# Optimization experiments

Measured on AMD Instinct MI355X. Metric: run time of the kernel, lower is better.

The kernel has to match this reference:

```python
import jax, jax.numpy as jnp
import numpy as np
from jax import lax

DIM = 192
HEADS = 8


def conv3d(x, w, b, groups=1, pad=0):
    # x: [B,C,T,H,W], w: [O, C//groups, kt, kh, kw]
    out = lax.conv_general_dilated(
        x, w, window_strides=(1, 1, 1),
        padding=[(pad, pad)] * 3,
        dimension_numbers=('NCDHW', 'OIDHW', 'NCDHW'),
        feature_group_count=groups)
    return out + b[None, :, None, None, None]


def setup_inputs() -> dict:
    key = jax.random.key(0)
    ks = jax.random.split(key, 8)
    d = DIM
    x = jax.random.normal(ks[0], (2, d, 8, 64, 64), dtype=jnp.float32)
    qkv_w = jax.random.normal(ks[1], (3 * d, d, 1, 1, 1), dtype=jnp.float32) * 0.02
    qkv_b = jnp.zeros((3 * d,), dtype=jnp.float32)
    dw_w = jax.random.normal(ks[2], (3 * d, 1, 3, 3, 3), dtype=jnp.float32) * 0.02
    dw_b = jnp.zeros((3 * d,), dtype=jnp.float32)
    temperature = jnp.ones((HEADS, 1, 1), dtype=jnp.float32)
    proj_w = jax.random.normal(ks[3], (d, d, 1, 1, 1), dtype=jnp.float32) * 0.02
    proj_b = jnp.zeros((d,), dtype=jnp.float32)
    return {"x": x, "qkv_w": qkv_w, "qkv_b": qkv_b, "dw_w": dw_w,
            "dw_b": dw_b, "temperature": temperature,
            "proj_w": proj_w, "proj_b": proj_b}


def reference(x, qkv_w, qkv_b, dw_w, dw_b, temperature, proj_w, proj_b):
    b, c, t, h, w = x.shape
    head_dim = c // HEADS
    n = t * h * w
    qkv = conv3d(x, qkv_w, qkv_b)                      # [b, 3c, t, h, w]
    qkv = conv3d(qkv, dw_w, dw_b, groups=3 * c, pad=1)  # depthwise 3x3x3
    q, k, v = jnp.split(qkv, 3, axis=1)
    def to_heads(z):
        return z.reshape(b, HEADS, head_dim, n)         # b head c (thw)
    q, k, v = to_heads(q), to_heads(k), to_heads(v)
    # L2 normalize along token axis (F.normalize, eps=1e-12)
    q = q / jnp.maximum(jnp.linalg.norm(q, axis=-1, keepdims=True), 1e-12)
    k = k / jnp.maximum(jnp.linalg.norm(k, axis=-1, keepdims=True), 1e-12)
    attn = jnp.einsum('bhcn,bhdn->bhcd', q, k) * temperature  # [b,H,hd,hd]
    attn = jax.nn.softmax(attn, axis=-1)
    out = jnp.einsum('bhcd,bhdn->bhcn', attn, v)        # [b,H,hd,n]
    out = out.reshape(b, c, t, h, w)
    return conv3d(out, proj_w, proj_b)
```

## Files before the change

### kernel.cpp

```cpp
#include <hip/hip_runtime.h>

#define NTOK 32768
#define CIN 192
#define C3 576
#define HEADS 8
#define HD 24

typedef __attribute__((ext_vector_type(8))) short bf16x8;
typedef __attribute__((ext_vector_type(16))) float f32x16;
typedef __attribute__((ext_vector_type(4))) unsigned int u32x4;

__device__ __forceinline__ float bf2f(unsigned int u) {
  union { unsigned int i; float f; } x; x.i = u << 16; return x.f;
}
__device__ __forceinline__ unsigned short f2bf(float f) {
  union { float f; unsigned int i; } x; x.f = f;
  unsigned int r = x.i + 0x7fffu + ((x.i >> 16) & 1u);
  return (unsigned short)(r >> 16);
}

__global__ __launch_bounds__(256) void k_wfrag(const float* __restrict__ W,
                                               unsigned short* __restrict__ Wf,
                                               int nchunk) {
  const int g = blockIdx.x * 256 + threadIdx.x;
  if (g >= nchunk) return;
  const int ol = g & 63, hi = (g >> 6) & 1, kk = (g >> 7) % 12, ot = g / 1536;
  const float* src = W + (size_t)(ot * 64 + ol) * CIN + kk * 16 + hi * 8;
  bf16x8 p;
#pragma unroll
  for (int e = 0; e < 8; ++e) p[e] = (short)f2bf(src[e]);
  *(bf16x8*)&Wf[(size_t)g * 8] = p;
}

__device__ __forceinline__ void issue12(bf16x8 (&a)[12],
                                        const unsigned short* p) {
#pragma unroll
  for (int kk = 0; kk < 12; ++kk) {
    unsigned long long ad = (unsigned long long)(p + kk * 1024);
    asm volatile("global_load_dwordx4 %0, %1, off" : "=v"(a[kk]) : "v"(ad));
  }
}

template<int XBF, int OUTF32>
__global__ __launch_bounds__(256, 2) void k_gemm_rr(
    const void* __restrict__ Xv, const unsigned short* __restrict__ Wf0,
    const float* __restrict__ bias, void* __restrict__ Yv, int ot_per,
    long xbs, long ybs, long wbs)
{
  __shared__ __align__(16) unsigned short Xf[12 * 128 * 8];
  const int tid = threadIdx.x;
  const int b = blockIdx.z;
  const int n0 = blockIdx.x * 64;
  const unsigned short* Wf = Wf0 + (size_t)b * wbs;
  const int lsub = tid & 15;

  if (XBF) {
    const unsigned short* X = (const unsigned short*)Xv + (size_t)b * xbs;
#pragma unroll
    for (int i = 0; i < 12; ++i) {
      const int g = tid + i * 256;
      const int c = g >> 4, nq = (g & 15) * 4;
      unsigned short t4[4];
      *(unsigned long long*)t4 =
          *(const unsigned long long*)&X[(size_t)c * NTOK + n0 + nq];
      const int chunk = (c >> 4) * 128 + ((c >> 3) & 1) * 64 + nq;
      const int e = c & 7;
#pragma unroll
      for (int s = 0; s < 4; ++s) {
        const int le = (s + lsub) & 3;
        Xf[(chunk + le) * 8 + e] = t4[le];
      }
    }
  } else {
    const float* X = (const float*)Xv + (size_t)b * xbs;
#pragma unroll
    for (int i = 0; i < 12; ++i) {
      const int g = tid + i * 256;
      const int c = g >> 4, nq = (g & 15) * 4;
      float4 v = *(const float4*)&X[(size_t)c * NTOK + n0 + nq];
      float vv[4] = {v.x, v.y, v.z, v.w};
      const int chunk = (c >> 4) * 128 + ((c >> 3) & 1) * 64 + nq;
      const int e = c & 7;
#pragma unroll
      for (int s = 0; s < 4; ++s) {
        const int le = (s + lsub) & 3;
        Xf[(chunk + le) * 8 + e] = f2bf(vv[le]);
      }
    }
  }
  __syncthreads();

  const int lane = tid & 63;
  const int wv = tid >> 6;
  const int o_w = (wv >> 1) * 32;
  const int n_w = (wv & 1) * 32;
  const int j = lane & 31;
  const int hi = lane >> 5;

  bf16x8 bfr[12];
#pragma unroll
  for (int kk = 0; kk < 12; ++kk)
    bfr[kk] = *(const bf16x8*)&Xf[(kk * 128 + hi * 64 + n_w + j) * 8];

  const unsigned short* wbase = Wf + ((size_t)hi * 64 + o_w + j) * 8;

  auto tile = [&](bf16x8 (&a)[12], int o0) {
    f32x16 acc0, acc1;
#pragma unroll
    for (int i = 0; i < 16; ++i) { acc0[i] = 0.f; acc1[i] = 0.f; }
#pragma unroll
    for (int kp = 0; kp < 6; ++kp) {
      acc0 = __builtin_amdgcn_mfma_f32_32x32x16_bf16(a[2 * kp], bfr[2 * kp], acc0, 0, 0, 0);
      acc1 = __builtin_amdgcn_mfma_f32_32x32x16_bf16(a[2 * kp + 1], bfr[2 * kp + 1], acc1, 0, 0, 0);
    }
    if (OUTF32) {
      float* Y = (float*)Yv + (size_t)b * ybs;
#pragma unroll
      for (int r = 0; r < 16; ++r) {
        const int row = o_w + (r & 3) + 8 * (r >> 2) + 4 * hi;
        Y[(size_t)(o0 + row) * NTOK + n0 + n_w + j] =
            acc0[r] + acc1[r] + bias[o0 + row];
      }
    } else {
      unsigned short* Y = (unsigned short*)Yv + (size_t)b * ybs;
#pragma unroll
      for (int r = 0; r < 16; ++r) {
        const int row = o_w + (r & 3) + 8 * (r >> 2) + 4 * hi;
        Y[(size_t)(o0 + row) * NTOK + n0 + n_w + j] =
            f2bf(acc0[r] + acc1[r] + bias[o0 + row]);
      }
    }
  };

  bf16x8 aA[12], aB[12];
  issue12(aA, wbase);
  asm volatile("s_waitcnt vmcnt(0)" ::: "memory");
  __builtin_amdgcn_sched_barrier(0);

  int it = 0;
  while (true) {
    if (it + 1 < ot_per) issue12(aB, wbase + (size_t)(it + 1) * 12288);
    tile(aA, it * 64);
    if (it + 1 >= ot_per) break;
    asm volatile("s_waitcnt vmcnt(16)" ::: "memory");
    __builtin_amdgcn_sched_barrier(0);
    ++it;
    if (it + 1 < ot_per) issue12(aA, wbase + (size_t)(it + 1) * 12288);
    tile(aB, it * 64);
    if (it + 1 >= ot_per) break;
    asm volatile("s_waitcnt vmcnt(16)" ::: "memory");
    __builtin_amdgcn_sched_barrier(0);
    ++it;
  }
}

__global__ __launch_bounds__(256, 2) void k_dwconv(
    const unsigned short* __restrict__ in0,
    const float* __restrict__ wdw,
    const float* __restrict__ bdw,
    unsigned short* __restrict__ out0)
{
  __shared__ __align__(16) unsigned short s[8][18][76];
  const int tid = threadIdx.x;
  const int ch = blockIdx.y;
  const int h0 = blockIdx.x * 16;
  const size_t boff = (size_t)blockIdx.z * C3 * NTOK;
  const unsigned short* inch = in0 + boff + (size_t)ch * NTOK;

  for (int r = tid; r < 144; r += 256) {
    const int t = r / 18, rr = r % 18;
    s[t][rr][7] = 0;
    s[t][rr][72] = 0;
  }
  for (int idx = tid; idx < 144 * 8; idx += 256) {
    const int row = idx >> 3, seg = idx & 7;
    const int t = row / 18, rr = row % 18;
    const int h = h0 + rr - 1;
    u32x4 v = {0u, 0u, 0u, 0u};
    if (h >= 0 && h < 64)
      v = *(const u32x4*)&inch[t * 4096 + h * 64 + seg * 8];
    *(u32x4*)&s[t][rr][8 + seg * 8] = v;
  }
  float wr[27];
#pragma unroll
  for (int i = 0; i < 27; ++i) wr[i] = wdw[ch * 27 + i];
  const float bias = bdw[ch];
  __syncthreads();

  const int wloc = tid & 63;
  const int hl0 = (tid >> 6) * 4;
  float acc[8][4];
#pragma unroll
  for (int t = 0; t < 8; ++t)
#pragma unroll
    for (int i = 0; i < 4; ++i) acc[t][i] = 0.f;

#pragma unroll
  for (int tt = 0; tt < 8; ++tt) {
    float v[6][3];
#pragma unroll
    for (int r = 0; r < 6; ++r)
#pragma unroll
      for (int c = 0; c < 3; ++c)
        v[r][c] = bf2f(s[tt][hl0 + r][7 + wloc + c]);
#pragma unroll
    for (int p = 0; p < 3; ++p) {
      const int t = tt + 1 - p;
      if (t < 0 || t > 7) continue;
#pragma unroll
      for (int hi = 0; hi < 4; ++hi) {
        float a = 0.f;
#pragma unroll
        for (int dh = 0; dh < 3; ++dh)
#pragma unroll
          for (int dw = 0; dw < 3; ++dw)
            a += wr[p * 9 + dh * 3 + dw] * v[hi + dh][dw];
        acc[t][hi] += a;
      }
    }
  }

  unsigned short* outch = out0 + boff + (size_t)ch * NTOK;
#pragma unroll
  for (int t = 0; t < 8; ++t)
#pragma unroll
    for (int hi = 0; hi < 4; ++hi)
      outch[t * 4096 + (h0 + hl0 + hi) * 64 + wloc] = f2bf(acc[t][hi] + bias);
}

__global__ __launch_bounds__(256) void k_gram(
    const unsigned short* __restrict__ post0, float* __restrict__ Sp0)
{
  const int tid = threadIdx.x;
  const int h = blockIdx.y;
  const unsigned short* post = post0 + (size_t)blockIdx.z * C3 * NTOK;
  float* Sp = Sp0 + (size_t)blockIdx.z * HEADS * 32 * 640;
  const int lane = tid & 63;
  const int wv = tid >> 6;
  const int c = lane & 31;
  const int off = (lane >> 5) * 8;
  const unsigned short* q = post + (size_t)(h * HD + c) * NTOK;
  const unsigned short* k = post + (size_t)(192 + h * HD + c) * NTOK;

  __shared__ float Sl[24][25];
  __shared__ float nl[48];
  for (int i = tid; i < 600; i += 256) ((float*)Sl)[i] = 0.f;
  if (tid < 48) nl[tid] = 0.f;
  __syncthreads();

  f32x16 acc;
#pragma unroll
  for (int i = 0; i < 16; ++i) acc[i] = 0.f;
  float sqq = 0.f, sqk = 0.f;

  const int base = blockIdx.x * 1024 + wv * 256 + off;
#pragma unroll
  for (int i = 0; i < 16; ++i) {
    const int n = base + i * 16;
    bf16x8 a = *(const bf16x8*)&q[n];
    bf16x8 b = *(const bf16x8*)&k[n];
#pragma unroll
    for (int e = 0; e < 8; ++e) {
      float fa = bf2f((unsigned short)a[e]);
      float fb = bf2f((unsigned short)b[e]);
      sqq += fa * fa;
      sqk += fb * fb;
    }
    acc = __builtin_amdgcn_mfma_f32_32x32x16_bf16(a, b, acc, 0, 0, 0);
  }

  sqq += __shfl_down(sqq, 32, 64);
  sqk += __shfl_down(sqk, 32, 64);
  if (lane < 32 && c < 24) {
    atomicAdd(&nl[c], sqq);
    atomicAdd(&nl[24 + c], sqk);
  }
  if (c < 24) {
#pragma unroll
    for (int r = 0; r < 16; ++r) {
      const int row = (r & 3) + 8 * (r >> 2) + 4 * (lane >> 5);
      if (row < 24) atomicAdd(&Sl[row][c], acc[r]);
    }
  }
  __syncthreads();
  float* outp = Sp + ((size_t)h * 32 + blockIdx.x) * 640;
  for (int i = tid; i < 576; i += 256) outp[i] = Sl[i / 24][i % 24];
  if (tid < 48) outp[576 + tid] = nl[tid];
}

__global__ __launch_bounds__(256) void k_attn_wfrag(
    const float* __restrict__ Sp0, const float* __restrict__ temp,
    const float* __restrict__ projw, unsigned short* __restrict__ wfc0)
{
  const int h = blockIdx.x;
  const int tid = threadIdx.x;
  const float* base = Sp0 + (size_t)blockIdx.y * HEADS * 32 * 640 +
                      (size_t)h * 32 * 640;
  unsigned short* wfc = wfc0 + (size_t)blockIdx.y * 3 * 1536 * 8;

  __shared__ float Ssum[24][25];
  __shared__ float attn[24][25];
  __shared__ float nqs[24], nks[24];

  for (int i = tid; i < 576; i += 256) {
    float a = 0.f;
#pragma unroll 4
    for (int ch = 0; ch < 32; ++ch) a += base[(size_t)ch * 640 + i];
    Ssum[i / 24][i % 24] = a;
  }
  if (tid < 48) {
    float a = 0.f;
#pragma unroll 4
    for (int ch = 0; ch < 32; ++ch) a += base[(size_t)ch * 640 + 576 + tid];
    float nv = fmaxf(sqrtf(a), 1e-12f);
    if (tid < 24) nqs[tid] = nv; else nks[tid - 24] = nv;
  }
  __syncthreads();
  if (tid < 24) {
    const int c = tid;
    const float tmp = temp[h];
    float row[24];
    float m = -1e30f;
#pragma unroll
    for (int d = 0; d < 24; ++d) {
      float v = Ssum[c][d] / (nqs[c] * nks[d]) * tmp;
      row[d] = v;
      m = fmaxf(m, v);
    }
    float ssum = 0.f;
#pragma unroll
    for (int d = 0; d < 24; ++d) { float e = __expf(row[d] - m); row[d] = e; ssum += e; }
    const float inv = 1.f / ssum;
#pragma unroll
    for (int d = 0; d < 24; ++d) attn[c][d] = row[d] * inv;
  }
  __syncthreads();
  for (int e = tid; e < 192 * 24; e += 256) {
    const int o = e / 24, d = e % 24;
    float a = 0.f;
#pragma unroll
    for (int c = 0; c < 24; ++c) a += projw[o * 192 + h * 24 + c] * attn[c][d];
    const int c2 = h * 24 + d;
    const int ot = o >> 6, ol = o & 63;
    const int kk = c2 >> 4, hi = (c2 >> 3) & 1, e2 = c2 & 7;
    wfc[(size_t)((((ot * 12 + kk) * 2 + hi) * 64) + ol) * 8 + e2] = f2bf(a);
  }
}

extern "C" void kernel_launch(void* const* d_in, const int* in_sizes, int n_in,
                              void* d_out, int out_size, void* d_ws, size_t ws_size,
                              hipStream_t stream) {
  const float* x      = (const float*)d_in[0];
  const float* qkv_w  = (const float*)d_in[1];
  const float* qkv_b  = (const float*)d_in[2];
  const float* dw_w   = (const float*)d_in[3];
  const float* dw_b   = (const float*)d_in[4];
  const float* temp   = (const float*)d_in[5];
  const float* proj_w = (const float*)d_in[6];
  const float* proj_b = (const float*)d_in[7];
  float* out = (float*)d_out;

  char* ws = (char*)d_ws;
  size_t off = 0;
  unsigned short* post = (unsigned short*)(ws + off);
  off += (size_t)2 * C3 * NTOK * sizeof(unsigned short);
  unsigned short* pre = (unsigned short*)(ws + off);
  off += (size_t)2 * C3 * NTOK * sizeof(unsigned short);
  float* Sp = (float*)(ws + off);
  off += (size_t)2 * HEADS * 32 * 640 * sizeof(float);
  off = (off + 255) & ~(size_t)255;
  unsigned short* wfq = (unsigned short*)(ws + off);
  off += (size_t)9 * 1536 * 8 * sizeof(unsigned short);
  unsigned short* wfc = (unsigned short*)(ws + off);
  off += (size_t)2 * 3 * 1536 * 8 * sizeof(unsigned short);

  k_wfrag<<<54, 256, 0, stream>>>(qkv_w, wfq, 9 * 1536);

  k_gemm_rr<0, 0><<<dim3(512, 1, 2), 256, 0, stream>>>(
      x, wfq, qkv_b, pre, 9, (long)CIN * NTOK, (long)C3 * NTOK, 0);

  k_dwconv<<<dim3(4, C3, 2), 256, 0, stream>>>(pre, dw_w, dw_b, post);

  k_gram<<<dim3(32, HEADS, 2), 256, 0, stream>>>(post, Sp);

  k_attn_wfrag<<<dim3(HEADS, 2), 256, 0, stream>>>(Sp, temp, proj_w, wfc);

  k_gemm_rr<1, 1><<<dim3(512, 1, 2), 256, 0, stream>>>(
      post + (size_t)384 * NTOK, wfc, proj_b, out, 3,
      (long)C3 * NTOK, (long)CIN * NTOK, (long)3 * 1536 * 8);
}
```

Baseline: 153.6 us.

## Split GEMM output channels across blocks with XCD-aware block remapping

Both pointwise GEMMs are relaunched with three times as many blocks. Each block now covers one third of the output-channel tiles (three tiles for the QKV GEMM, one for the projection) instead of all of them. Block IDs are remapped so the three blocks sharing a token tile land on the same XCD and can reuse the X tile in that XCD's L2. This raises parallelism and shortens per-block serial work, but each block still loads and converts the full X tile into shared memory, so X staging work triples.

```diff
diff --git a/kernel.cpp b/kernel.cpp
--- a/kernel.cpp
+++ b/kernel.cpp
@@ -41,16 +41,21 @@
   }
 }
 
-template<int XBF, int OUTF32>
+template<int XBF, int OUTF32, int OT>
 __global__ __launch_bounds__(256, 2) void k_gemm_rr(
     const void* __restrict__ Xv, const unsigned short* __restrict__ Wf0,
-    const float* __restrict__ bias, void* __restrict__ Yv, int ot_per,
+    const float* __restrict__ bias, void* __restrict__ Yv,
     long xbs, long ybs, long wbs)
 {
   __shared__ __align__(16) unsigned short Xf[12 * 128 * 8];
   const int tid = threadIdx.x;
-  const int b = blockIdx.z;
-  const int n0 = blockIdx.x * 64;
+  const int bid = blockIdx.x;
+  const int xcd = bid & 7;
+  const int kb = bid >> 3;
+  const int oc = kb % 3;
+  const int g2 = xcd * 128 + kb / 3;
+  const int n0 = (g2 & 511) * 64;
+  const int b = g2 >> 9;
   const unsigned short* Wf = Wf0 + (size_t)b * wbs;
   const int lsub = tid & 15;
 
@@ -102,7 +107,9 @@
   for (int kk = 0; kk < 12; ++kk)
     bfr[kk] = *(const bf16x8*)&Xf[(kk * 128 + hi * 64 + n_w + j) * 8];
 
-  const unsigned short* wbase = Wf + ((size_t)hi * 64 + o_w + j) * 8;
+  const int ob = oc * OT * 64;
+  const unsigned short* wbase =
+      Wf + ((size_t)(oc * OT) * 1536 + hi * 64 + o_w + j) * 8;
 
   auto tile = [&](bf16x8 (&a)[12], int o0) {
     f32x16 acc0, acc1;
@@ -137,20 +144,18 @@
   asm volatile("s_waitcnt vmcnt(0)" ::: "memory");
   __builtin_amdgcn_sched_barrier(0);
 
-  int it = 0;
-  while (true) {
-    if (it + 1 < ot_per) issue12(aB, wbase + (size_t)(it + 1) * 12288);
-    tile(aA, it * 64);
-    if (it + 1 >= ot_per) break;
+  if (OT == 1) {
+    tile(aA, ob);
+  } else {
+    issue12(aB, wbase + 12288);
+    tile(aA, ob);
     asm volatile("s_waitcnt vmcnt(16)" ::: "memory");
     __builtin_amdgcn_sched_barrier(0);
-    ++it;
-    if (it + 1 < ot_per) issue12(aA, wbase + (size_t)(it + 1) * 12288);
-    tile(aB, it * 64);
-    if (it + 1 >= ot_per) break;
+    issue12(aA, wbase + 24576);
+    tile(aB, ob + 64);
     asm volatile("s_waitcnt vmcnt(16)" ::: "memory");
     __builtin_amdgcn_sched_barrier(0);
-    ++it;
+    tile(aA, ob + 128);
   }
 }
 
@@ -376,8 +381,8 @@
 
   k_wfrag<<<54, 256, 0, stream>>>(qkv_w, wfq, 9 * 1536);
 
-  k_gemm_rr<0, 0><<<dim3(512, 1, 2), 256, 0, stream>>>(
-      x, wfq, qkv_b, pre, 9, (long)CIN * NTOK, (long)C3 * NTOK, 0);
+  k_gemm_rr<0, 0, 3><<<3072, 256, 0, stream>>>(
+      x, wfq, qkv_b, pre, (long)CIN * NTOK, (long)C3 * NTOK, 0);
 
   k_dwconv<<<dim3(4, C3, 2), 256, 0, stream>>>(pre, dw_w, dw_b, post);
 
@@ -385,7 +390,7 @@
 
   k_attn_wfrag<<<dim3(HEADS, 2), 256, 0, stream>>>(Sp, temp, proj_w, wfc);
 
-  k_gemm_rr<1, 1><<<dim3(512, 1, 2), 256, 0, stream>>>(
-      post + (size_t)384 * NTOK, wfc, proj_b, out, 3,
+  k_gemm_rr<1, 1, 1><<<3072, 256, 0, stream>>>(
+      post + (size_t)384 * NTOK, wfc, proj_b, out,
       (long)C3 * NTOK, (long)CIN * NTOK, (long)3 * 1536 * 8);
 }
```

New measurement: 150.7 us. Within noise of the previous version (-1.9%).

## Run depthwise 3D conv on MFMA via banded weight matrices, simplify GEMM X staging

Applied to the files above, without the earlier changes.

The depthwise 3x3x3 conv is recast as matrix multiplies. Banded bf16 weight fragments along the h axis are built per channel and applied with 32x32x16 MFMAs over a transposed LDS tile (w-major, h-padded). This is meant to move the stencil FMAs from scalar ALU onto the matrix cores, at the cost of wasted MFMA work on zeros and scalar 16-bit LDS writes during staging. The GEMM kernel also stores X in a plain padded row-major LDS tile and gathers B fragments with per-element LDS reads instead of a pre-swizzled layout. That makes staging simpler but the fragment reads costlier.

```diff
diff --git a/kernel.cpp b/kernel.cpp
--- a/kernel.cpp
+++ b/kernel.cpp
@@ -47,12 +47,11 @@
     const float* __restrict__ bias, void* __restrict__ Yv, int ot_per,
     long xbs, long ybs, long wbs)
 {
-  __shared__ __align__(16) unsigned short Xf[12 * 128 * 8];
+  __shared__ __align__(16) unsigned short Xl[192][68];
   const int tid = threadIdx.x;
   const int b = blockIdx.z;
   const int n0 = blockIdx.x * 64;
   const unsigned short* Wf = Wf0 + (size_t)b * wbs;
-  const int lsub = tid & 15;
 
   if (XBF) {
     const unsigned short* X = (const unsigned short*)Xv + (size_t)b * xbs;
@@ -60,16 +59,8 @@
     for (int i = 0; i < 12; ++i) {
       const int g = tid + i * 256;
       const int c = g >> 4, nq = (g & 15) * 4;
-      unsigned short t4[4];
-      *(unsigned long long*)t4 =
+      *(unsigned long long*)&Xl[c][nq] =
           *(const unsigned long long*)&X[(size_t)c * NTOK + n0 + nq];
-      const int chunk = (c >> 4) * 128 + ((c >> 3) & 1) * 64 + nq;
-      const int e = c & 7;
-#pragma unroll
-      for (int s = 0; s < 4; ++s) {
-        const int le = (s + lsub) & 3;
-        Xf[(chunk + le) * 8 + e] = t4[le];
-      }
     }
   } else {
     const float* X = (const float*)Xv + (size_t)b * xbs;
@@ -78,14 +69,8 @@
       const int g = tid + i * 256;
       const int c = g >> 4, nq = (g & 15) * 4;
       float4 v = *(const float4*)&X[(size_t)c * NTOK + n0 + nq];
-      float vv[4] = {v.x, v.y, v.z, v.w};
-      const int chunk = (c >> 4) * 128 + ((c >> 3) & 1) * 64 + nq;
-      const int e = c & 7;
-#pragma unroll
-      for (int s = 0; s < 4; ++s) {
-        const int le = (s + lsub) & 3;
-        Xf[(chunk + le) * 8 + e] = f2bf(vv[le]);
-      }
+      unsigned short p[4] = {f2bf(v.x), f2bf(v.y), f2bf(v.z), f2bf(v.w)};
+      *(unsigned long long*)&Xl[c][nq] = *(unsigned long long*)p;
     }
   }
   __syncthreads();
@@ -100,7 +85,9 @@
   bf16x8 bfr[12];
 #pragma unroll
   for (int kk = 0; kk < 12; ++kk)
-    bfr[kk] = *(const bf16x8*)&Xf[(kk * 128 + hi * 64 + n_w + j) * 8];
+#pragma unroll
+    for (int e = 0; e < 8; ++e)
+      bfr[kk][e] = (short)Xl[kk * 16 + hi * 8 + e][n_w + j];
 
   const unsigned short* wbase = Wf + ((size_t)hi * 64 + o_w + j) * 8;
 
@@ -154,78 +141,110 @@
   }
 }
 
-__global__ __launch_bounds__(256, 2) void k_dwconv(
+__global__ __launch_bounds__(256, 2) void k_dwconv_mfma(
     const unsigned short* __restrict__ in0,
     const float* __restrict__ wdw,
     const float* __restrict__ bdw,
     unsigned short* __restrict__ out0)
 {
-  __shared__ __align__(16) unsigned short s[8][18][76];
+  __shared__ __align__(16) unsigned short S[8][34][72];
   const int tid = threadIdx.x;
+  const int wblk = blockIdx.x;
   const int ch = blockIdx.y;
-  const int h0 = blockIdx.x * 16;
   const size_t boff = (size_t)blockIdx.z * C3 * NTOK;
   const unsigned short* inch = in0 + boff + (size_t)ch * NTOK;
 
-  for (int r = tid; r < 144; r += 256) {
-    const int t = r / 18, rr = r % 18;
-    s[t][rr][7] = 0;
-    s[t][rr][72] = 0;
-  }
-  for (int idx = tid; idx < 144 * 8; idx += 256) {
-    const int row = idx >> 3, seg = idx & 7;
-    const int t = row / 18, rr = row % 18;
-    const int h = h0 + rr - 1;
-    u32x4 v = {0u, 0u, 0u, 0u};
-    if (h >= 0 && h < 64)
-      v = *(const u32x4*)&inch[t * 4096 + h * 64 + seg * 8];
-    *(u32x4*)&s[t][rr][8 + seg * 8] = v;
-  }
-  float wr[27];
-#pragma unroll
-  for (int i = 0; i < 27; ++i) wr[i] = wdw[ch * 27 + i];
+  for (int idx = tid; idx < 8 * 34 * 8; idx += 256) {
+    const int t = idx / 272;
+    const int rem = idx % 272;
+    const int wl = rem >> 3;
+    const int z = rem & 7;
+    const int hl = (z == 0) ? 0 : 64 + z;
+    S[t][wl][hl] = 0;
+  }
+  {
+    const int wg0 = wblk * 32 - 2;
+#pragma unroll
+    for (int rr = 0; rr < 2; ++rr) {
+      const int r = tid * 2 + rr;
+      const int t = r >> 6, h = r & 63;
+      const unsigned short* rowp = inch + t * 4096 + h * 64;
+#pragma unroll
+      for (int u = 0; u < 18; ++u) {
+        const int w = wg0 + 2 * u;
+        unsigned int pv = 0;
+        if (w >= 0 && w <= 62) pv = *(const unsigned int*)&rowp[w];
+        const int wl0 = 2 * u - 1;
+        if (wl0 >= 0)  S[t][wl0][h + 1]     = (unsigned short)(pv & 0xffffu);
+        if (wl0 < 33)  S[t][wl0 + 1][h + 1] = (unsigned short)(pv >> 16);
+      }
+    }
+  }
+
+  const int lane = tid & 63;
+  const int wv = tid >> 6;
+  const int H = wv & 1;
+  const int tq = wv >> 1;
+  const int j32 = lane & 31;
+  const int kg = lane >> 5;
   const float bias = bdw[ch];
-  __syncthreads();
-
-  const int wloc = tid & 63;
-  const int hl0 = (tid >> 6) * 4;
-  float acc[8][4];
-#pragma unroll
-  for (int t = 0; t < 8; ++t)
-#pragma unroll
-    for (int i = 0; i < 4; ++i) acc[t][i] = 0.f;
-
-#pragma unroll
-  for (int tt = 0; tt < 8; ++tt) {
-    float v[6][3];
-#pragma unroll
-    for (int r = 0; r < 6; ++r)
-#pragma unroll
-      for (int c = 0; c < 3; ++c)
-        v[r][c] = bf2f(s[tt][hl0 + r][7 + wloc + c]);
-#pragma unroll
-    for (int p = 0; p < 3; ++p) {
-      const int t = tt + 1 - p;
-      if (t < 0 || t > 7) continue;
-#pragma unroll
-      for (int hi = 0; hi < 4; ++hi) {
-        float a = 0.f;
-#pragma unroll
-        for (int dh = 0; dh < 3; ++dh)
-#pragma unroll
-          for (int dw = 0; dw < 3; ++dw)
-            a += wr[p * 9 + dh * 3 + dw] * v[hi + dh][dw];
-        acc[t][hi] += a;
+
+  float K[27];
+#pragma unroll
+  for (int q = 0; q < 27; ++q) K[q] = wdw[ch * 27 + q];
+  bf16x8 Afr[27];
+#pragma unroll
+  for (int dt = 0; dt < 3; ++dt)
+#pragma unroll
+    for (int dw = 0; dw < 3; ++dw)
+#pragma unroll
+      for (int s = 0; s < 3; ++s) {
+        bf16x8 pk;
+#pragma unroll
+        for (int e = 0; e < 8; ++e) {
+          const int k = kg * 8 + e;
+          int dh; bool use;
+          if (s == 0)      { dh = k - j32;      use = (dh >= 0 && dh <= 2); }
+          else if (s == 1) { dh = k + 16 - j32; use = (dh >= 0 && dh <= 2); }
+          else             { dh = k + 24 - j32; use = (dh >= 0 && dh <= 2) && (k >= 8); }
+          unsigned short v = 0;
+          if (use) v = f2bf(K[dt * 9 + dh * 3 + dw]);
+          pk[e] = (short)v;
+        }
+        Afr[dt * 9 + dw * 3 + s] = pk;
       }
-    }
-  }
-
-  unsigned short* outch = out0 + boff + (size_t)ch * NTOK;
-#pragma unroll
-  for (int t = 0; t < 8; ++t)
-#pragma unroll
-    for (int hi = 0; hi < 4; ++hi)
-      outch[t * 4096 + (h0 + hl0 + hi) * 64 + wloc] = f2bf(acc[t][hi] + bias);
+  __syncthreads();
+
+  for (int t = tq * 4; t < tq * 4 + 4; ++t) {
+    f32x16 accP, accQ;
+#pragma unroll
+    for (int i = 0; i < 16; ++i) { accP[i] = 0.f; accQ[i] = 0.f; }
+
+#pragma unroll
+    for (int dt = 0; dt < 3; ++dt) {
+      const int tin = t + dt - 1;
+      if (tin < 0 || tin > 7) continue;
+#pragma unroll
+      for (int dw = 0; dw < 3; ++dw) {
+        const unsigned short* bp = &S[tin][j32 + dw][0];
+#pragma unroll
+        for (int s = 0; s < 3; ++s) {
+          const int sb = (s == 0) ? 0 : (s == 1 ? 16 : 24);
+          bf16x8 b = *(const bf16x8*)(bp + 32 * H + sb + kg * 8);
+          if ((dw * 3 + s) & 1)
+            accQ = __builtin_amdgcn_mfma_f32_32x32x16_bf16(Afr[dt * 9 + dw * 3 + s], b, accQ, 0, 0, 0);
+          else
+            accP = __builtin_amdgcn_mfma_f32_32x32x16_bf16(Afr[dt * 9 + dw * 3 + s], b, accP, 0, 0, 0);
+        }
+      }
+    }
+    unsigned short* outp = out0 + boff + (size_t)ch * NTOK + t * 4096 + wblk * 32 + j32;
+#pragma unroll
+    for (int r = 0; r < 16; ++r) {
+      const int hrow = 32 * H + (r & 3) + 8 * (r >> 2) + 4 * kg;
+      outp[hrow * 64] = f2bf(accP[r] + accQ[r] + bias);
+    }
+  }
 }
 
 __global__ __launch_bounds__(256) void k_gram(
@@ -379,7 +398,7 @@
   k_gemm_rr<0, 0><<<dim3(512, 1, 2), 256, 0, stream>>>(
       x, wfq, qkv_b, pre, 9, (long)CIN * NTOK, (long)C3 * NTOK, 0);
 
-  k_dwconv<<<dim3(4, C3, 2), 256, 0, stream>>>(pre, dw_w, dw_b, post);
+  k_dwconv_mfma<<<dim3(2, C3, 2), 256, 0, stream>>>(pre, dw_w, dw_b, post);
 
   k_gram<<<dim3(32, HEADS, 2), 256, 0, stream>>>(post, Sp);
 
```

New measurement: 327.8 us. +113.4%, slower.
